# Performance work log

Hardware: AMD Instinct MI355X
Metric: run time of the kernel (lower is better)

The kernel has to match this reference:

```python
import jax, jax.numpy as jnp
import numpy as np

B = 32768
H = 320          # pred_hidden
V = 34           # num_classes
BLANK = V - 1    # padding_idx for embedding


def setup_inputs() -> dict:
    key = jax.random.key(0)
    ks = jax.random.split(key, 12)
    s = 0.05
    embed_W = jax.random.normal(ks[0], (V, H), jnp.float32) * s
    embed_W = embed_W.at[BLANK].set(0.0)  # padding_idx row is zeros in torch
    return {
        "x": jax.random.randint(ks[1], (B,), 0, V, jnp.int32),
        "enc_proj_line": jax.random.normal(ks[2], (B, H), jnp.float32),
        "h": jax.random.normal(ks[3], (1, B, H), jnp.float32),
        "c": jax.random.normal(ks[4], (1, B, H), jnp.float32),
        "embed_W": embed_W,
        "W_ih": jax.random.normal(ks[5], (4 * H, H), jnp.float32) * s,
        "W_hh": jax.random.normal(ks[6], (4 * H, H), jnp.float32) * s,
        "b_ih": jax.random.normal(ks[7], (4 * H,), jnp.float32) * s,
        "b_hh": jax.random.normal(ks[8], (4 * H,), jnp.float32) * s,
        "pred_W": jax.random.normal(ks[9], (H, H), jnp.float32) * s,
        "pred_b": jnp.zeros((H,), jnp.float32),
        "joint_W": jax.random.normal(ks[10], (V, H), jnp.float32) * s,
        "joint_b": jnp.zeros((V,), jnp.float32),
    }


def reference(x, enc_proj_line, h, c, embed_W, W_ih, W_hh, b_ih, b_hh,
              pred_W, pred_b, joint_W, joint_b):
    # embedding lookup: [B, H]
    emb = embed_W[x]
    # single-timestep LSTM cell (torch gate order: i, f, g, o)
    gates = emb @ W_ih.T + b_ih + h[0] @ W_hh.T + b_hh  # [B, 4H]
    i, f, g, o = jnp.split(gates, 4, axis=-1)
    i = jax.nn.sigmoid(i)
    f = jax.nn.sigmoid(f)
    g = jnp.tanh(g)
    o = jax.nn.sigmoid(o)
    c_new = f * c[0] + i * g                 # [B, H]
    h_new = o * jnp.tanh(c_new)              # [B, H] == g[0] (lstm output)
    # pred projection + joint
    pred_proj = h_new @ pred_W.T + pred_b    # [B, H]
    joint_out = (enc_proj_line + pred_proj) @ joint_W.T + joint_b  # [B, V]
    dec = jnp.argmax(joint_out, axis=-1)
    return dec, h_new[None], c_new[None]
```

## Files before the change

### kernel.cpp

```cpp
#include <hip/hip_runtime.h>
#include <math.h>

#define NB 32768
#define H 320
#define V 34
#define N4 1280
#define BM 128
#define BN 128
#define BK 32
#define KSTEPS (H / BK)
#define NWG ((NB / BM) * (N4 / BN))

typedef _Float16 f16;
typedef f16 f16x4 __attribute__((ext_vector_type(4)));
typedef f16 f16x8 __attribute__((ext_vector_type(8)));
typedef float f32x4 __attribute__((ext_vector_type(4)));

#define WS_GTP 0
#define WS_C2 43520
#define WS_JB2 54400
#define WS_HALF_BYTE 217744
#define WP_COUNT (N4 * H)
#define WS_JP_BYTE 1856144
#define JP_COUNT (48 * 640)
#define BUILD_T0 43520
#define BUILD_T1 54400
#define BUILD_T2 54434
#define BUILD_TOTAL (BUILD_T2 + WP_COUNT)

#define JBM 64
#define JBN 48
#define JBK 32
#define JKSTEPS 20

__device__ __forceinline__ float sigf(float x) {
    return 1.0f / (1.0f + __expf(-x));
}
__device__ __forceinline__ float tanh_fast(float x) {
    return 1.0f - 2.0f / (1.0f + __expf(2.0f * x));
}

__global__ void build_tables(const float* __restrict__ embed_W,
                             const float* __restrict__ W_ih,
                             const float* __restrict__ b_ih,
                             const float* __restrict__ b_hh,
                             const float* __restrict__ pred_W,
                             const float* __restrict__ pred_b,
                             const float* __restrict__ joint_W,
                             const float* __restrict__ joint_b,
                             const float* __restrict__ W_hh,
                             float* __restrict__ ws) {
    int tid = blockIdx.x * blockDim.x + threadIdx.x;
    if (tid < BUILD_T0) {
        int v = tid / N4, n = tid % N4;
        int orig = (n & 3) * H + (n >> 2);
        float acc = b_ih[orig] + b_hh[orig];
        const float* e = embed_W + (size_t)v * H;
        const float* w = W_ih + (size_t)orig * H;
        for (int k = 0; k < H; k += 4) {
            float4 e4 = *(const float4*)(e + k);
            float4 w4 = *(const float4*)(w + k);
            acc = fmaf(e4.x, w4.x, acc);
            acc = fmaf(e4.y, w4.y, acc);
            acc = fmaf(e4.z, w4.z, acc);
            acc = fmaf(e4.w, w4.w, acc);
        }
        ws[WS_GTP + tid] = acc;
    } else if (tid < BUILD_T1) {
        int idx = tid - BUILD_T0;
        int v = idx / H, k = idx % H;
        float acc = 0.0f;
        for (int j = 0; j < H; ++j)
            acc = fmaf(joint_W[(size_t)v * H + j], pred_W[(size_t)j * H + k], acc);
        ws[tid] = acc;
    } else if (tid < BUILD_T2) {
        int v = tid - BUILD_T1;
        float acc = joint_b[v];
        for (int j = 0; j < H; ++j)
            acc = fmaf(joint_W[(size_t)v * H + j], pred_b[j], acc);
        ws[tid] = acc;
    } else if (tid < BUILD_TOTAL) {
        int idx = tid - BUILD_T2;
        int n = idx / H, k = idx % H;
        int orig = (n & 3) * H + (n >> 2);
        float wv = W_hh[(size_t)orig * H + k];
        f16 w1 = (f16)wv;
        f16 w2 = (f16)((wv - (float)w1) * 2048.0f);
        f16* wp1 = (f16*)((char*)ws + WS_HALF_BYTE);
        wp1[idx] = w1;
        wp1[WP_COUNT + idx] = w2;
    }
}

__global__ void build_joint(const float* __restrict__ joint_W,
                            float* __restrict__ ws) {
    int tid = blockIdx.x * blockDim.x + threadIdx.x;
    if (tid >= JP_COUNT) return;
    int n = tid / 640, k = tid % 640;
    float wv = 0.0f;
    if (n < V)
        wv = (k < H) ? joint_W[(size_t)n * H + k] : ws[WS_C2 + (size_t)n * H + (k - H)];
    f16 w1 = (f16)wv;
    f16 w2 = (f16)((wv - (float)w1) * 2048.0f);
    f16* jp1 = (f16*)((char*)ws + WS_JP_BYTE);
    jp1[tid] = w1;
    jp1[JP_COUNT + tid] = w2;
}

__device__ __forceinline__ void stage_tile(int w, int lane, int m0, int n0, int kc,
                                           const float* __restrict__ h_in,
                                           const f16* __restrict__ Wp1,
                                           const f16* __restrict__ Wp2,
                                           f16* A1, f16* A2, f16* B1, f16* B2) {
    #pragma unroll
    for (int i = 0; i < 4; ++i) {
        int r = (w * 4 + i) * 8 + (lane >> 3);
        int cf = (lane & 7) * 4;
        float4 hv = *(const float4*)(h_in + (size_t)(m0 + r) * H + kc + cf);
        f16x4 h1v, h2v;
        f16 a;
        a = (f16)hv.x; h1v[0] = a; h2v[0] = (f16)((hv.x - (float)a) * 2048.0f);
        a = (f16)hv.y; h1v[1] = a; h2v[1] = (f16)((hv.y - (float)a) * 2048.0f);
        a = (f16)hv.z; h1v[2] = a; h2v[2] = (f16)((hv.z - (float)a) * 2048.0f);
        a = (f16)hv.w; h1v[3] = a; h2v[3] = (f16)((hv.w - (float)a) * 2048.0f);
        *(f16x4*)(A1 + r * 32 + cf) = h1v;
        *(f16x4*)(A2 + r * 32 + cf) = h2v;
    }
    #pragma unroll
    for (int i = 0; i < 2; ++i) {
        int nrow = (w * 2 + i) * 16 + (lane >> 2);
        int kh = (lane & 3) * 8;
        *(int4*)(B1 + nrow * 32 + kh) =
            *(const int4*)(Wp1 + (size_t)(n0 + nrow) * H + kc + kh);
        *(int4*)(B2 + nrow * 32 + kh) =
            *(const int4*)(Wp2 + (size_t)(n0 + nrow) * H + kc + kh);
    }
}

__launch_bounds__(256, 2)
__global__ void lstm_gemm(const int* __restrict__ x,
                          const float* __restrict__ h_in,
                          const float* __restrict__ c_in,
                          const float* __restrict__ ws,
                          float* __restrict__ out) {
    __shared__ __align__(16) char smem[65536];
    const int tid = threadIdx.x, lane = tid & 63, w = tid >> 6;

    int l = (blockIdx.x & 7) * (NWG / 8) + (blockIdx.x >> 3);
    const int mb = l / (N4 / BN);
    const int nb = l % (N4 / BN);
    const int m0 = mb * BM, n0 = nb * BN;

    const f16* Wp1 = (const f16*)((const char*)ws + WS_HALF_BYTE);
    const f16* Wp2 = Wp1 + WP_COUNT;
    const float* gtp = ws + WS_GTP;
    float* hn_out = out + NB;
    float* cn_out = out + NB + (size_t)NB * H;

    f16* base = (f16*)smem;

    f32x4 accM[4][4], accC[4][4];
    #pragma unroll
    for (int i = 0; i < 4; ++i)
        #pragma unroll
        for (int j = 0; j < 4; ++j) {
            accM[i][j] = (f32x4){0.f, 0.f, 0.f, 0.f};
            accC[i][j] = (f32x4){0.f, 0.f, 0.f, 0.f};
        }

    stage_tile(w, lane, m0, n0, 0, h_in, Wp1, Wp2,
               base, base + 4096, base + 8192, base + 12288);
    __syncthreads();

    const int wm = (w >> 1) * 64, wn = (w & 1) * 64;
    int cur = 0;
    for (int t = 0; t < KSTEPS; ++t) {
        if (t < KSTEPS - 1) {
            f16* nb_ = base + (cur ^ 1) * 16384;
            stage_tile(w, lane, m0, n0, (t + 1) * BK, h_in, Wp1, Wp2,
                       nb_, nb_ + 4096, nb_ + 8192, nb_ + 12288);
        }
        f16* A1 = base + cur * 16384;
        f16* A2 = A1 + 4096;
        f16* B1 = A1 + 8192;
        f16* B2 = A1 + 12288;
        const int ar = (lane & 15) * 32 + (lane >> 4) * 8;

        f16x8 a[4], b1[4], b2[4];
        #pragma unroll
        for (int mi = 0; mi < 4; ++mi)
            a[mi] = *(const f16x8*)(A1 + (wm + mi * 16) * 32 + ar);
        #pragma unroll
        for (int nj = 0; nj < 4; ++nj)
            b1[nj] = *(const f16x8*)(B1 + (wn + nj * 16) * 32 + ar);
        #pragma unroll
        for (int mi = 0; mi < 4; ++mi)
            #pragma unroll
            for (int nj = 0; nj < 4; ++nj)
                accM[mi][nj] = __builtin_amdgcn_mfma_f32_16x16x32_f16(
                    a[mi], b1[nj], accM[mi][nj], 0, 0, 0);
        #pragma unroll
        for (int nj = 0; nj < 4; ++nj)
            b2[nj] = *(const f16x8*)(B2 + (wn + nj * 16) * 32 + ar);
        #pragma unroll
        for (int mi = 0; mi < 4; ++mi)
            #pragma unroll
            for (int nj = 0; nj < 4; ++nj)
                accC[mi][nj] = __builtin_amdgcn_mfma_f32_16x16x32_f16(
                    a[mi], b2[nj], accC[mi][nj], 0, 0, 0);
        #pragma unroll
        for (int mi = 0; mi < 4; ++mi)
            a[mi] = *(const f16x8*)(A2 + (wm + mi * 16) * 32 + ar);
        #pragma unroll
        for (int mi = 0; mi < 4; ++mi)
            #pragma unroll
            for (int nj = 0; nj < 4; ++nj)
                accC[mi][nj] = __builtin_amdgcn_mfma_f32_16x16x32_f16(
                    a[mi], b1[nj], accC[mi][nj], 0, 0, 0);
        __syncthreads();
        cur ^= 1;
    }

    float* gates = (float*)smem;
    #pragma unroll
    for (int mi = 0; mi < 4; ++mi)
        #pragma unroll
        for (int nj = 0; nj < 4; ++nj) {
            f32x4 vm = accM[mi][nj];
            f32x4 vc = accC[mi][nj];
            int n = wn + nj * 16 + (lane & 15);
            int mb4 = wm + mi * 16 + (lane >> 4) * 4;
            #pragma unroll
            for (int q = 0; q < 4; ++q)
                gates[(mb4 + q) * 128 + n] = fmaf(vc[q], 1.0f / 2048.0f, vm[q]);
        }
    __syncthreads();

    const int hk0 = n0 >> 2;
    #pragma unroll 4
    for (int it = 0; it < 16; ++it) {
        int idx = it * 256 + tid;
        int ml = idx >> 5, hkl = idx & 31;
        f32x4 g4 = *(const f32x4*)&gates[ml * 128 + hkl * 4];
        int m = m0 + ml;
        int hk = hk0 + hkl;
        int xv = x[m];
        float4 b4 = *(const float4*)(gtp + (size_t)xv * N4 + n0 + hkl * 4);
        float ig = sigf(g4[0] + b4.x);
        float fg = sigf(g4[1] + b4.y);
        float gg = tanh_fast(g4[2] + b4.z);
        float og = sigf(g4[3] + b4.w);
        float cv = c_in[(size_t)m * H + hk];
        float cn = fmaf(fg, cv, ig * gg);
        float hn = og * tanh_fast(cn);
        hn_out[(size_t)m * H + hk] = hn;
        cn_out[(size_t)m * H + hk] = cn;
    }
}

__launch_bounds__(256, 2)
__global__ void joint_argmax(const float* __restrict__ enc,
                             const float* __restrict__ ws,
                             float* __restrict__ out) {
    __shared__ __align__(16) char smem[28672];
    const int tid = threadIdx.x, lane = tid & 63, w = tid >> 6;
    const int m0 = blockIdx.x * JBM;

    const f16* Jp1 = (const f16*)((const char*)ws + WS_JP_BYTE);
    const f16* Jp2 = Jp1 + JP_COUNT;
    const float* hn = out + NB;
    const float* jb2 = ws + WS_JB2;

    f16* base = (f16*)smem;

    f32x4 accM[3], accC[3];
    #pragma unroll
    for (int j = 0; j < 3; ++j) {
        accM[j] = (f32x4){0.f, 0.f, 0.f, 0.f};
        accC[j] = (f32x4){0.f, 0.f, 0.f, 0.f};
    }

    auto stage = [&](int t, f16* A1, f16* A2, f16* B1, f16* B2) {
        const float* src = (t < 10) ? enc : hn;
        const int off = (t % 10) * JBK;
        #pragma unroll
        for (int i = 0; i < 2; ++i) {
            int r = (w * 2 + i) * 8 + (lane >> 3);
            int cf = (lane & 7) * 4;
            float4 hv = *(const float4*)(src + (size_t)(m0 + r) * H + off + cf);
            f16x4 h1v, h2v;
            f16 a;
            a = (f16)hv.x; h1v[0] = a; h2v[0] = (f16)((hv.x - (float)a) * 2048.0f);
            a = (f16)hv.y; h1v[1] = a; h2v[1] = (f16)((hv.y - (float)a) * 2048.0f);
            a = (f16)hv.z; h1v[2] = a; h2v[2] = (f16)((hv.z - (float)a) * 2048.0f);
            a = (f16)hv.w; h1v[3] = a; h2v[3] = (f16)((hv.w - (float)a) * 2048.0f);
            *(f16x4*)(A1 + r * 32 + cf) = h1v;
            *(f16x4*)(A2 + r * 32 + cf) = h2v;
        }
        if (tid < 192) {
            int n = tid >> 2, kh = (tid & 3) * 8;
            size_t gsrc = (size_t)n * 640 + t * JBK + kh;
            *(int4*)(B1 + n * 32 + kh) = *(const int4*)(Jp1 + gsrc);
            *(int4*)(B2 + n * 32 + kh) = *(const int4*)(Jp2 + gsrc);
        }
    };

    stage(0, base, base + 2048, base + 4096, base + 5632);
    __syncthreads();

    const int wm = w * 16;
    int cur = 0;
    for (int t = 0; t < JKSTEPS; ++t) {
        if (t < JKSTEPS - 1) {
            f16* nb_ = base + (cur ^ 1) * 7168;
            stage(t + 1, nb_, nb_ + 2048, nb_ + 4096, nb_ + 5632);
        }
        f16* A1 = base + cur * 7168;
        f16* A2 = A1 + 2048;
        f16* B1 = A1 + 4096;
        f16* B2 = A1 + 5632;
        const int ar = (lane & 15) * 32 + (lane >> 4) * 8;

        f16x8 a1 = *(const f16x8*)(A1 + wm * 32 + ar);
        f16x8 a2 = *(const f16x8*)(A2 + wm * 32 + ar);
        f16x8 b1[3], b2[3];
        #pragma unroll
        for (int nj = 0; nj < 3; ++nj) {
            b1[nj] = *(const f16x8*)(B1 + nj * 16 * 32 + ar);
            b2[nj] = *(const f16x8*)(B2 + nj * 16 * 32 + ar);
        }
        #pragma unroll
        for (int nj = 0; nj < 3; ++nj) {
            accM[nj] = __builtin_amdgcn_mfma_f32_16x16x32_f16(a1, b1[nj], accM[nj], 0, 0, 0);
            accC[nj] = __builtin_amdgcn_mfma_f32_16x16x32_f16(a1, b2[nj], accC[nj], 0, 0, 0);
            accC[nj] = __builtin_amdgcn_mfma_f32_16x16x32_f16(a2, b1[nj], accC[nj], 0, 0, 0);
        }
        __syncthreads();
        cur ^= 1;
    }

    float* lg = (float*)smem;
    #pragma unroll
    for (int nj = 0; nj < 3; ++nj) {
        int n = nj * 16 + (lane & 15);
        int mr = wm + (lane >> 4) * 4;
        #pragma unroll
        for (int q = 0; q < 4; ++q)
            lg[(mr + q) * 49 + n] = fmaf(accC[nj][q], 1.0f / 2048.0f, accM[nj][q]);
    }
    __syncthreads();

    if (tid < JBM) {
        const float* row = lg + tid * 49;
        float best = row[0] + jb2[0];
        int bi = 0;
        #pragma unroll
        for (int v = 1; v < V; ++v) {
            float t2 = row[v] + jb2[v];
            if (t2 > best) { best = t2; bi = v; }
        }
        out[m0 + tid] = (float)bi;
    }
}

extern "C" void kernel_launch(void* const* d_in, const int* in_sizes, int n_in,
                              void* d_out, int out_size, void* d_ws, size_t ws_size,
                              hipStream_t stream) {
    const int*   x       = (const int*)  d_in[0];
    const float* enc     = (const float*)d_in[1];
    const float* h       = (const float*)d_in[2];
    const float* c       = (const float*)d_in[3];
    const float* embed_W = (const float*)d_in[4];
    const float* W_ih    = (const float*)d_in[5];
    const float* W_hh    = (const float*)d_in[6];
    const float* b_ih    = (const float*)d_in[7];
    const float* b_hh    = (const float*)d_in[8];
    const float* pred_W  = (const float*)d_in[9];
    const float* pred_b  = (const float*)d_in[10];
    const float* joint_W = (const float*)d_in[11];
    const float* joint_b = (const float*)d_in[12];
    float* out = (float*)d_out;
    float* ws  = (float*)d_ws;

    int tblocks = (BUILD_TOTAL + 255) / 256;
    build_tables<<<tblocks, 256, 0, stream>>>(embed_W, W_ih, b_ih, b_hh,
                                              pred_W, pred_b, joint_W, joint_b,
                                              W_hh, ws);
    build_joint<<<(JP_COUNT + 255) / 256, 256, 0, stream>>>(joint_W, ws);
    lstm_gemm<<<NWG, 256, 0, stream>>>(x, h, c, ws, out);
    joint_argmax<<<NB / JBM, 256, 0, stream>>>(enc, ws, out);
}
```

Baseline: 166.0 us.

## Pre-split h into tiled fp16 pairs and stage GEMM tiles via global_load_lds

Adds a split_h kernel that converts h into hi/lo fp16 pairs once, stored in a tile-contiguous layout in the workspace. W_hh is also stored tile-contiguous. A new lstm_gemm_fast kernel stages A and B tiles straight into LDS with global_load_lds, with each wave copying one contiguous 8KB block, so the GEMM no longer converts fp32 to fp16 per tile or goes through registers. The cost is an extra kernel launch plus writing and re-reading about 42MB of split h. The fast path is used only when the workspace is large enough, otherwise the old kernel runs.

```diff
diff --git a/kernel.cpp b/kernel.cpp
--- a/kernel.cpp
+++ b/kernel.cpp
@@ -19,14 +19,18 @@
 #define WS_GTP 0
 #define WS_C2 43520
 #define WS_JB2 54400
-#define WS_HALF_BYTE 217744
-#define WP_COUNT (N4 * H)
+#define WS_B_BYTE 217744
+#define BT_COUNT (N4 * H)
 #define WS_JP_BYTE 1856144
 #define JP_COUNT (48 * 640)
+#define WS_AT_BYTE 1979136
+#define AT_COUNT (NB * H)
+#define FAST_WS_NEED (WS_AT_BYTE + 2ull * AT_COUNT * 2)
+
 #define BUILD_T0 43520
 #define BUILD_T1 54400
 #define BUILD_T2 54434
-#define BUILD_TOTAL (BUILD_T2 + WP_COUNT)
+#define BUILD_TOTAL (BUILD_T2 + BT_COUNT)
 
 #define JBM 64
 #define JBN 48
@@ -39,6 +43,9 @@
 __device__ __forceinline__ float tanh_fast(float x) {
     return 1.0f - 2.0f / (1.0f + __expf(2.0f * x));
 }
+
+typedef const __attribute__((address_space(1))) unsigned int* gas_t;
+typedef __attribute__((address_space(3))) unsigned int* las_t;
 
 __global__ void build_tables(const float* __restrict__ embed_W,
                              const float* __restrict__ W_ih,
@@ -86,9 +93,10 @@
         float wv = W_hh[(size_t)orig * H + k];
         f16 w1 = (f16)wv;
         f16 w2 = (f16)((wv - (float)w1) * 2048.0f);
-        f16* wp1 = (f16*)((char*)ws + WS_HALF_BYTE);
-        wp1[idx] = w1;
-        wp1[WP_COUNT + idx] = w2;
+        int off = ((n >> 7) * KSTEPS + (k >> 5)) * 4096 + (n & 127) * 32 + (k & 31);
+        f16* bt1 = (f16*)((char*)ws + WS_B_BYTE);
+        bt1[off] = w1;
+        bt1[BT_COUNT + off] = w2;
     }
 }
 
@@ -107,11 +115,161 @@
     jp1[JP_COUNT + tid] = w2;
 }
 
-__device__ __forceinline__ void stage_tile(int w, int lane, int m0, int n0, int kc,
+__global__ void split_h(const float* __restrict__ h_in, float* __restrict__ ws) {
+    int tid = blockIdx.x * blockDim.x + threadIdx.x;
+    int e = tid * 4;
+    int m = e / H, k = e % H;
+    float4 hv = *(const float4*)(h_in + e);
+    f16x4 h1v, h2v;
+    f16 a;
+    a = (f16)hv.x; h1v[0] = a; h2v[0] = (f16)((hv.x - (float)a) * 2048.0f);
+    a = (f16)hv.y; h1v[1] = a; h2v[1] = (f16)((hv.y - (float)a) * 2048.0f);
+    a = (f16)hv.z; h1v[2] = a; h2v[2] = (f16)((hv.z - (float)a) * 2048.0f);
+    a = (f16)hv.w; h1v[3] = a; h2v[3] = (f16)((hv.w - (float)a) * 2048.0f);
+    int off = ((m >> 7) * KSTEPS + (k >> 5)) * 4096 + (m & 127) * 32 + (k & 31);
+    f16* at1 = (f16*)((char*)ws + WS_AT_BYTE);
+    *(f16x4*)(at1 + off) = h1v;
+    *(f16x4*)(at1 + AT_COUNT + off) = h2v;
+}
+
+__launch_bounds__(256, 2)
+__global__ void lstm_gemm_fast(const int* __restrict__ x,
+                               const float* __restrict__ c_in,
+                               const float* __restrict__ ws,
+                               float* __restrict__ out) {
+    __shared__ __align__(16) char smem[65536];
+    const int tid = threadIdx.x, lane = tid & 63, w = tid >> 6;
+
+    int l = (blockIdx.x & 7) * (NWG / 8) + (blockIdx.x >> 3);
+    const int mb = l / (N4 / BN);
+    const int nb = l % (N4 / BN);
+    const int m0 = mb * BM, n0 = nb * BN;
+
+    const f16* At1 = (const f16*)((const char*)ws + WS_AT_BYTE);
+    const f16* Bt1 = (const f16*)((const char*)ws + WS_B_BYTE);
+    const float* gtp = ws + WS_GTP;
+    float* hn_out = out + NB;
+    float* cn_out = out + NB + (size_t)NB * H;
+
+    f32x4 accM[4][4], accC[4][4];
+    #pragma unroll
+    for (int i = 0; i < 4; ++i)
+        #pragma unroll
+        for (int j = 0; j < 4; ++j) {
+            accM[i][j] = (f32x4){0.f, 0.f, 0.f, 0.f};
+            accC[i][j] = (f32x4){0.f, 0.f, 0.f, 0.f};
+        }
+
+    auto stage = [&](int ks, int buf) {
+        const f16* src;
+        if (w == 0)      src = At1 + (size_t)(mb * KSTEPS + ks) * 4096;
+        else if (w == 1) src = At1 + AT_COUNT + (size_t)(mb * KSTEPS + ks) * 4096;
+        else if (w == 2) src = Bt1 + (size_t)(nb * KSTEPS + ks) * 4096;
+        else             src = Bt1 + BT_COUNT + (size_t)(nb * KSTEPS + ks) * 4096;
+        char* ldst = smem + buf * 32768 + w * 8192;
+        #pragma unroll
+        for (int i = 0; i < 8; ++i) {
+            __builtin_amdgcn_global_load_lds(
+                (gas_t)(const void*)(src + i * 512 + lane * 8),
+                (las_t)(void*)(ldst + i * 1024), 16, 0, 0);
+        }
+    };
+
+    stage(0, 0);
+    __syncthreads();
+
+    const int wm = (w >> 1) * 64, wn = (w & 1) * 64;
+    const int ar = (lane & 15) * 32 + (lane >> 4) * 8;
+    int cur = 0;
+    for (int t = 0; t < KSTEPS; ++t) {
+        if (t < KSTEPS - 1) stage(t + 1, cur ^ 1);
+        const f16* A1 = (const f16*)(smem + cur * 32768);
+        const f16* A2 = A1 + 4096;
+        const f16* B1 = A1 + 8192;
+        const f16* B2 = A1 + 12288;
+
+        f16x8 a[4], b1[4], b2[4];
+        #pragma unroll
+        for (int mi = 0; mi < 4; ++mi)
+            a[mi] = *(const f16x8*)(A1 + (wm + mi * 16) * 32 + ar);
+        #pragma unroll
+        for (int nj = 0; nj < 4; ++nj)
+            b1[nj] = *(const f16x8*)(B1 + (wn + nj * 16) * 32 + ar);
+        #pragma unroll
+        for (int mi = 0; mi < 4; ++mi)
+            #pragma unroll
+            for (int nj = 0; nj < 4; ++nj)
+                accM[mi][nj] = __builtin_amdgcn_mfma_f32_16x16x32_f16(
+                    a[mi], b1[nj], accM[mi][nj], 0, 0, 0);
+        #pragma unroll
+        for (int nj = 0; nj < 4; ++nj)
+            b2[nj] = *(const f16x8*)(B2 + (wn + nj * 16) * 32 + ar);
+        #pragma unroll
+        for (int mi = 0; mi < 4; ++mi)
+            #pragma unroll
+            for (int nj = 0; nj < 4; ++nj)
+                accC[mi][nj] = __builtin_amdgcn_mfma_f32_16x16x32_f16(
+                    a[mi], b2[nj], accC[mi][nj], 0, 0, 0);
+        #pragma unroll
+        for (int mi = 0; mi < 4; ++mi)
+            a[mi] = *(const f16x8*)(A2 + (wm + mi * 16) * 32 + ar);
+        #pragma unroll
+        for (int mi = 0; mi < 4; ++mi)
+            #pragma unroll
+            for (int nj = 0; nj < 4; ++nj)
+                accC[mi][nj] = __builtin_amdgcn_mfma_f32_16x16x32_f16(
+                    a[mi], b1[nj], accC[mi][nj], 0, 0, 0);
+        __syncthreads();
+        cur ^= 1;
+    }
+
+    float* gates = (float*)smem;
+    #pragma unroll
+    for (int mi = 0; mi < 4; ++mi)
+        #pragma unroll
+        for (int nj = 0; nj < 4; ++nj) {
+            f32x4 vm = accM[mi][nj];
+            f32x4 vc = accC[mi][nj];
+            int n = wn + nj * 16 + (lane & 15);
+            int mb4 = wm + mi * 16 + (lane >> 4) * 4;
+            #pragma unroll
+            for (int q = 0; q < 4; ++q) {
+                int row = mb4 + q;
+                gates[row * 128 + (n ^ ((row & 7) << 2))] =
+                    fmaf(vc[q], 1.0f / 2048.0f, vm[q]);
+            }
+        }
+    __syncthreads();
+
+    const int hk0 = n0 >> 2;
+    #pragma unroll 4
+    for (int it = 0; it < 16; ++it) {
+        int idx = it * 256 + tid;
+        int ml = idx >> 5, hkl = idx & 31;
+        int k0 = (ml & 7) << 2;
+        f32x4 g4 = *(const f32x4*)&gates[ml * 128 + ((hkl * 4) ^ k0)];
+        int m = m0 + ml;
+        int hk = hk0 + hkl;
+        int xv = x[m];
+        float4 b4 = *(const float4*)(gtp + (size_t)xv * N4 + n0 + hkl * 4);
+        float ig = sigf(g4[0] + b4.x);
+        float fg = sigf(g4[1] + b4.y);
+        float gg = tanh_fast(g4[2] + b4.z);
+        float og = sigf(g4[3] + b4.w);
+        float cv = c_in[(size_t)m * H + hk];
+        float cn = fmaf(fg, cv, ig * gg);
+        float hn = og * tanh_fast(cn);
+        hn_out[(size_t)m * H + hk] = hn;
+        cn_out[(size_t)m * H + hk] = cn;
+    }
+}
+
+__device__ __forceinline__ void stage_tile(int w, int lane, int m0, int nb, int ks,
                                            const float* __restrict__ h_in,
-                                           const f16* __restrict__ Wp1,
-                                           const f16* __restrict__ Wp2,
+                                           const f16* __restrict__ Bt1,
+                                           const f16* __restrict__ Bt2,
                                            f16* A1, f16* A2, f16* B1, f16* B2) {
+    int kc = ks * BK;
     #pragma unroll
     for (int i = 0; i < 4; ++i) {
         int r = (w * 4 + i) * 8 + (lane >> 3);
@@ -130,10 +288,9 @@
     for (int i = 0; i < 2; ++i) {
         int nrow = (w * 2 + i) * 16 + (lane >> 2);
         int kh = (lane & 3) * 8;
-        *(int4*)(B1 + nrow * 32 + kh) =
-            *(const int4*)(Wp1 + (size_t)(n0 + nrow) * H + kc + kh);
-        *(int4*)(B2 + nrow * 32 + kh) =
-            *(const int4*)(Wp2 + (size_t)(n0 + nrow) * H + kc + kh);
+        size_t src = (size_t)(nb * KSTEPS + ks) * 4096 + nrow * 32 + kh;
+        *(int4*)(B1 + nrow * 32 + kh) = *(const int4*)(Bt1 + src);
+        *(int4*)(B2 + nrow * 32 + kh) = *(const int4*)(Bt2 + src);
     }
 }
 
@@ -151,8 +308,8 @@
     const int nb = l % (N4 / BN);
     const int m0 = mb * BM, n0 = nb * BN;
 
-    const f16* Wp1 = (const f16*)((const char*)ws + WS_HALF_BYTE);
-    const f16* Wp2 = Wp1 + WP_COUNT;
+    const f16* Bt1 = (const f16*)((const char*)ws + WS_B_BYTE);
+    const f16* Bt2 = Bt1 + BT_COUNT;
     const float* gtp = ws + WS_GTP;
     float* hn_out = out + NB;
     float* cn_out = out + NB + (size_t)NB * H;
@@ -168,7 +325,7 @@
             accC[i][j] = (f32x4){0.f, 0.f, 0.f, 0.f};
         }
 
-    stage_tile(w, lane, m0, n0, 0, h_in, Wp1, Wp2,
+    stage_tile(w, lane, m0, nb, 0, h_in, Bt1, Bt2,
                base, base + 4096, base + 8192, base + 12288);
     __syncthreads();
 
@@ -177,7 +334,7 @@
     for (int t = 0; t < KSTEPS; ++t) {
         if (t < KSTEPS - 1) {
             f16* nb_ = base + (cur ^ 1) * 16384;
-            stage_tile(w, lane, m0, n0, (t + 1) * BK, h_in, Wp1, Wp2,
+            stage_tile(w, lane, m0, nb, t + 1, h_in, Bt1, Bt2,
                        nb_, nb_ + 4096, nb_ + 8192, nb_ + 12288);
         }
         f16* A1 = base + cur * 16384;
@@ -387,6 +544,12 @@
                                               pred_W, pred_b, joint_W, joint_b,
                                               W_hh, ws);
     build_joint<<<(JP_COUNT + 255) / 256, 256, 0, stream>>>(joint_W, ws);
-    lstm_gemm<<<NWG, 256, 0, stream>>>(x, h, c, ws, out);
+
+    if (ws_size >= FAST_WS_NEED) {
+        split_h<<<(AT_COUNT / 4) / 256, 256, 0, stream>>>(h, ws);
+        lstm_gemm_fast<<<NWG, 256, 0, stream>>>(x, c, ws, out);
+    } else {
+        lstm_gemm<<<NWG, 256, 0, stream>>>(x, h, c, ws, out);
+    }
     joint_argmax<<<NB / JBM, 256, 0, stream>>>(enc, ws, out);
 }
```

New measurement: 171.2 us. +3.1%, slower.

## Pre-split h and W_hh into MFMA-tiled fp16 layouts, stage via global_load_lds

Applied to the files above, without the earlier changes.

A merged prep kernel now splits h and W_hh into hi/lo fp16 pairs, stored in tile-contiguous layouts that match the MFMA fragment order. The LSTM GEMM then stages tiles straight into LDS with global_load_lds, so it no longer converts in-loop or issues register round-trips. It also folds build_joint into prep, swizzles the gate scratch in LDS to avoid bank conflicts, and retiles the joint weight layout. The trade-off is an extra full pass over h (write and reread of 2x fp16 copies, about 42MB) in exchange for a simpler, faster main loop.

```diff
diff --git a/kernel.cpp b/kernel.cpp
--- a/kernel.cpp
+++ b/kernel.cpp
@@ -17,22 +17,24 @@
 typedef float f32x4 __attribute__((ext_vector_type(4)));
 
 #define WS_GTP 0
-#define WS_C2 43520
 #define WS_JB2 54400
-#define WS_HALF_BYTE 217744
-#define WP_COUNT (N4 * H)
+#define WS_B_BYTE 217744
+#define BT_COUNT (N4 * H)
 #define WS_JP_BYTE 1856144
 #define JP_COUNT (48 * 640)
-#define BUILD_T0 43520
-#define BUILD_T1 54400
-#define BUILD_T2 54434
-#define BUILD_TOTAL (BUILD_T2 + WP_COUNT)
+#define WS_AT_BYTE 1979136
+#define AT_COUNT (NB * H)
 
 #define JBM 64
-#define JBN 48
 #define JBK 32
 #define JKSTEPS 20
 
+#define PREP_P4 1280
+#define PREP_P2 50
+#define PREP_P0 170
+#define PREP_P3 120
+#define PREP_NWG (PREP_P4 + PREP_P2 + PREP_P0 + PREP_P3 + 1)
+
 __device__ __forceinline__ float sigf(float x) {
     return 1.0f / (1.0f + __expf(-x));
 }
@@ -40,19 +42,71 @@
     return 1.0f - 2.0f / (1.0f + __expf(2.0f * x));
 }
 
-__global__ void build_tables(const float* __restrict__ embed_W,
-                             const float* __restrict__ W_ih,
-                             const float* __restrict__ b_ih,
-                             const float* __restrict__ b_hh,
-                             const float* __restrict__ pred_W,
-                             const float* __restrict__ pred_b,
-                             const float* __restrict__ joint_W,
-                             const float* __restrict__ joint_b,
-                             const float* __restrict__ W_hh,
-                             float* __restrict__ ws) {
-    int tid = blockIdx.x * blockDim.x + threadIdx.x;
-    if (tid < BUILD_T0) {
-        int v = tid / N4, n = tid % N4;
+typedef const __attribute__((address_space(1))) unsigned int* gas_t;
+typedef __attribute__((address_space(3))) unsigned int* las_t;
+
+__device__ __forceinline__ void split8(const float* e, f16x8& p1, f16x8& p2) {
+    #pragma unroll
+    for (int j = 0; j < 8; ++j) {
+        f16 a = (f16)e[j];
+        p1[j] = a;
+        p2[j] = (f16)((e[j] - (float)a) * 2048.0f);
+    }
+}
+
+__global__ void prep(const float* __restrict__ embed_W,
+                     const float* __restrict__ W_ih,
+                     const float* __restrict__ b_ih,
+                     const float* __restrict__ b_hh,
+                     const float* __restrict__ pred_W,
+                     const float* __restrict__ pred_b,
+                     const float* __restrict__ joint_W,
+                     const float* __restrict__ joint_b,
+                     const float* __restrict__ W_hh,
+                     const float* __restrict__ h_in,
+                     float* __restrict__ ws) {
+    const int bid = blockIdx.x;
+    const int t = threadIdx.x;
+    if (bid < PREP_P4) {
+        int id = bid * 256 + t;
+        int ks = id >> 15, m = id & 32767;
+        const float* src = h_in + (size_t)m * H + ks * 32;
+        f16* at1 = (f16*)((char*)ws + WS_AT_BYTE);
+        f16* at2 = at1 + AT_COUNT;
+        size_t tbase = ((size_t)(m >> 7) * KSTEPS + ks) * 4096
+                       + ((m & 127) >> 4) * 512 + (m & 15) * 8;
+        #pragma unroll
+        for (int g = 0; g < 4; ++g) {
+            float4 v0 = *(const float4*)(src + g * 8);
+            float4 v1 = *(const float4*)(src + g * 8 + 4);
+            float e[8] = {v0.x, v0.y, v0.z, v0.w, v1.x, v1.y, v1.z, v1.w};
+            f16x8 p1, p2;
+            split8(e, p1, p2);
+            *(f16x8*)(at1 + tbase + g * 128) = p1;
+            *(f16x8*)(at2 + tbase + g * 128) = p2;
+        }
+    } else if (bid < PREP_P4 + PREP_P2) {
+        int id = (bid - PREP_P4) * 256 + t;
+        int ks = id / 1280, n = id - ks * 1280;
+        int orig = (n & 3) * H + (n >> 2);
+        const float* src = W_hh + (size_t)orig * H + ks * 32;
+        f16* bt1 = (f16*)((char*)ws + WS_B_BYTE);
+        f16* bt2 = bt1 + BT_COUNT;
+        size_t tbase = ((size_t)(n >> 7) * KSTEPS + ks) * 4096
+                       + ((n & 127) >> 4) * 512 + (n & 15) * 8;
+        #pragma unroll
+        for (int g = 0; g < 4; ++g) {
+            float4 v0 = *(const float4*)(src + g * 8);
+            float4 v1 = *(const float4*)(src + g * 8 + 4);
+            float e[8] = {v0.x, v0.y, v0.z, v0.w, v1.x, v1.y, v1.z, v1.w};
+            f16x8 p1, p2;
+            split8(e, p1, p2);
+            *(f16x8*)(bt1 + tbase + g * 128) = p1;
+            *(f16x8*)(bt2 + tbase + g * 128) = p2;
+        }
+    } else if (bid < PREP_P4 + PREP_P2 + PREP_P0) {
+        int id = (bid - PREP_P4 - PREP_P2) * 256 + t;
+        int v = id / N4, n = id % N4;
         int orig = (n & 3) * H + (n >> 2);
         float acc = b_ih[orig] + b_hh[orig];
         const float* e = embed_W + (size_t)v * H;
@@ -65,84 +119,46 @@
             acc = fmaf(e4.z, w4.z, acc);
             acc = fmaf(e4.w, w4.w, acc);
         }
-        ws[WS_GTP + tid] = acc;
-    } else if (tid < BUILD_T1) {
-        int idx = tid - BUILD_T0;
-        int v = idx / H, k = idx % H;
-        float acc = 0.0f;
-        for (int j = 0; j < H; ++j)
-            acc = fmaf(joint_W[(size_t)v * H + j], pred_W[(size_t)j * H + k], acc);
-        ws[tid] = acc;
-    } else if (tid < BUILD_T2) {
-        int v = tid - BUILD_T1;
-        float acc = joint_b[v];
-        for (int j = 0; j < H; ++j)
-            acc = fmaf(joint_W[(size_t)v * H + j], pred_b[j], acc);
-        ws[tid] = acc;
-    } else if (tid < BUILD_TOTAL) {
-        int idx = tid - BUILD_T2;
-        int n = idx / H, k = idx % H;
-        int orig = (n & 3) * H + (n >> 2);
-        float wv = W_hh[(size_t)orig * H + k];
+        ws[WS_GTP + id] = acc;
+    } else if (bid < PREP_P4 + PREP_P2 + PREP_P0 + PREP_P3) {
+        int id = (bid - PREP_P4 - PREP_P2 - PREP_P0) * 256 + t;
+        int n = id / 640, k = id % 640;
+        float wv = 0.0f;
+        if (n < V) {
+            if (k < H) {
+                wv = joint_W[(size_t)n * H + k];
+            } else {
+                float acc = 0.0f;
+                const float* jw = joint_W + (size_t)n * H;
+                for (int j = 0; j < H; ++j)
+                    acc = fmaf(jw[j], pred_W[(size_t)j * H + (k - H)], acc);
+                wv = acc;
+            }
+        }
         f16 w1 = (f16)wv;
         f16 w2 = (f16)((wv - (float)w1) * 2048.0f);
-        f16* wp1 = (f16*)((char*)ws + WS_HALF_BYTE);
-        wp1[idx] = w1;
-        wp1[WP_COUNT + idx] = w2;
-    }
-}
-
-__global__ void build_joint(const float* __restrict__ joint_W,
-                            float* __restrict__ ws) {
-    int tid = blockIdx.x * blockDim.x + threadIdx.x;
-    if (tid >= JP_COUNT) return;
-    int n = tid / 640, k = tid % 640;
-    float wv = 0.0f;
-    if (n < V)
-        wv = (k < H) ? joint_W[(size_t)n * H + k] : ws[WS_C2 + (size_t)n * H + (k - H)];
-    f16 w1 = (f16)wv;
-    f16 w2 = (f16)((wv - (float)w1) * 2048.0f);
-    f16* jp1 = (f16*)((char*)ws + WS_JP_BYTE);
-    jp1[tid] = w1;
-    jp1[JP_COUNT + tid] = w2;
-}
-
-__device__ __forceinline__ void stage_tile(int w, int lane, int m0, int n0, int kc,
-                                           const float* __restrict__ h_in,
-                                           const f16* __restrict__ Wp1,
-                                           const f16* __restrict__ Wp2,
-                                           f16* A1, f16* A2, f16* B1, f16* B2) {
-    #pragma unroll
-    for (int i = 0; i < 4; ++i) {
-        int r = (w * 4 + i) * 8 + (lane >> 3);
-        int cf = (lane & 7) * 4;
-        float4 hv = *(const float4*)(h_in + (size_t)(m0 + r) * H + kc + cf);
-        f16x4 h1v, h2v;
-        f16 a;
-        a = (f16)hv.x; h1v[0] = a; h2v[0] = (f16)((hv.x - (float)a) * 2048.0f);
-        a = (f16)hv.y; h1v[1] = a; h2v[1] = (f16)((hv.y - (float)a) * 2048.0f);
-        a = (f16)hv.z; h1v[2] = a; h2v[2] = (f16)((hv.z - (float)a) * 2048.0f);
-        a = (f16)hv.w; h1v[3] = a; h2v[3] = (f16)((hv.w - (float)a) * 2048.0f);
-        *(f16x4*)(A1 + r * 32 + cf) = h1v;
-        *(f16x4*)(A2 + r * 32 + cf) = h2v;
-    }
-    #pragma unroll
-    for (int i = 0; i < 2; ++i) {
-        int nrow = (w * 2 + i) * 16 + (lane >> 2);
-        int kh = (lane & 3) * 8;
-        *(int4*)(B1 + nrow * 32 + kh) =
-            *(const int4*)(Wp1 + (size_t)(n0 + nrow) * H + kc + kh);
-        *(int4*)(B2 + nrow * 32 + kh) =
-            *(const int4*)(Wp2 + (size_t)(n0 + nrow) * H + kc + kh);
+        int kk = k & 31;
+        int off = (k >> 5) * 1536 + (n >> 4) * 512 + (kk >> 3) * 128
+                  + (n & 15) * 8 + (kk & 7);
+        f16* jp1 = (f16*)((char*)ws + WS_JP_BYTE);
+        jp1[off] = w1;
+        jp1[JP_COUNT + off] = w2;
+    } else {
+        if (t < V) {
+            float acc = joint_b[t];
+            const float* jw = joint_W + (size_t)t * H;
+            for (int j = 0; j < H; ++j)
+                acc = fmaf(jw[j], pred_b[j], acc);
+            ws[WS_JB2 + t] = acc;
+        }
     }
 }
 
 __launch_bounds__(256, 2)
-__global__ void lstm_gemm(const int* __restrict__ x,
-                          const float* __restrict__ h_in,
-                          const float* __restrict__ c_in,
-                          const float* __restrict__ ws,
-                          float* __restrict__ out) {
+__global__ void lstm_gemm_fast(const int* __restrict__ x,
+                               const float* __restrict__ c_in,
+                               const float* __restrict__ ws,
+                               float* __restrict__ out) {
     __shared__ __align__(16) char smem[65536];
     const int tid = threadIdx.x, lane = tid & 63, w = tid >> 6;
 
@@ -151,14 +167,12 @@
     const int nb = l % (N4 / BN);
     const int m0 = mb * BM, n0 = nb * BN;
 
-    const f16* Wp1 = (const f16*)((const char*)ws + WS_HALF_BYTE);
-    const f16* Wp2 = Wp1 + WP_COUNT;
+    const f16* At1 = (const f16*)((const char*)ws + WS_AT_BYTE);
+    const f16* Bt1 = (const f16*)((const char*)ws + WS_B_BYTE);
     const float* gtp = ws + WS_GTP;
     float* hn_out = out + NB;
     float* cn_out = out + NB + (size_t)NB * H;
 
-    f16* base = (f16*)smem;
-
     f32x4 accM[4][4], accC[4][4];
     #pragma unroll
     for (int i = 0; i < 4; ++i)
@@ -168,31 +182,42 @@
             accC[i][j] = (f32x4){0.f, 0.f, 0.f, 0.f};
         }
 
-    stage_tile(w, lane, m0, n0, 0, h_in, Wp1, Wp2,
-               base, base + 4096, base + 8192, base + 12288);
+    auto stage = [&](int ks, int buf) {
+        const f16* src;
+        if (w == 0)      src = At1 + (size_t)(mb * KSTEPS + ks) * 4096;
+        else if (w == 1) src = At1 + AT_COUNT + (size_t)(mb * KSTEPS + ks) * 4096;
+        else if (w == 2) src = Bt1 + (size_t)(nb * KSTEPS + ks) * 4096;
+        else             src = Bt1 + BT_COUNT + (size_t)(nb * KSTEPS + ks) * 4096;
+        char* ldst = smem + buf * 32768 + w * 8192;
+        #pragma unroll
+        for (int i = 0; i < 8; ++i) {
+            __builtin_amdgcn_global_load_lds(
+                (gas_t)(const void*)(src + i * 512 + lane * 8),
+                (las_t)(void*)(ldst + i * 1024), 16, 0, 0);
+        }
+    };
+
+    stage(0, 0);
     __syncthreads();
 
-    const int wm = (w >> 1) * 64, wn = (w & 1) * 64;
+    const int asub = (w >> 1) * 4;
+    const int bsub = (w & 1) * 4;
+    const int lo = lane * 8;
     int cur = 0;
     for (int t = 0; t < KSTEPS; ++t) {
-        if (t < KSTEPS - 1) {
-            f16* nb_ = base + (cur ^ 1) * 16384;
-            stage_tile(w, lane, m0, n0, (t + 1) * BK, h_in, Wp1, Wp2,
-                       nb_, nb_ + 4096, nb_ + 8192, nb_ + 12288);
-        }
-        f16* A1 = base + cur * 16384;
-        f16* A2 = A1 + 4096;
-        f16* B1 = A1 + 8192;
-        f16* B2 = A1 + 12288;
-        const int ar = (lane & 15) * 32 + (lane >> 4) * 8;
+        if (t < KSTEPS - 1) stage(t + 1, cur ^ 1);
+        const f16* A1 = (const f16*)(smem + cur * 32768);
+        const f16* A2 = A1 + 4096;
+        const f16* B1 = A1 + 8192;
+        const f16* B2 = A1 + 12288;
 
         f16x8 a[4], b1[4], b2[4];
         #pragma unroll
         for (int mi = 0; mi < 4; ++mi)
-            a[mi] = *(const f16x8*)(A1 + (wm + mi * 16) * 32 + ar);
+            a[mi] = *(const f16x8*)(A1 + (asub + mi) * 512 + lo);
         #pragma unroll
         for (int nj = 0; nj < 4; ++nj)
-            b1[nj] = *(const f16x8*)(B1 + (wn + nj * 16) * 32 + ar);
+            b1[nj] = *(const f16x8*)(B1 + (bsub + nj) * 512 + lo);
         #pragma unroll
         for (int mi = 0; mi < 4; ++mi)
             #pragma unroll
@@ -201,7 +226,7 @@
                     a[mi], b1[nj], accM[mi][nj], 0, 0, 0);
         #pragma unroll
         for (int nj = 0; nj < 4; ++nj)
-            b2[nj] = *(const f16x8*)(B2 + (wn + nj * 16) * 32 + ar);
+            b2[nj] = *(const f16x8*)(B2 + (bsub + nj) * 512 + lo);
         #pragma unroll
         for (int mi = 0; mi < 4; ++mi)
             #pragma unroll
@@ -210,7 +235,7 @@
                     a[mi], b2[nj], accC[mi][nj], 0, 0, 0);
         #pragma unroll
         for (int mi = 0; mi < 4; ++mi)
-            a[mi] = *(const f16x8*)(A2 + (wm + mi * 16) * 32 + ar);
+            a[mi] = *(const f16x8*)(A2 + (asub + mi) * 512 + lo);
         #pragma unroll
         for (int mi = 0; mi < 4; ++mi)
             #pragma unroll
@@ -221,6 +246,7 @@
         cur ^= 1;
     }
 
+    const int wm = (w >> 1) * 64, wn = (w & 1) * 64;
     float* gates = (float*)smem;
     #pragma unroll
     for (int mi = 0; mi < 4; ++mi)
@@ -231,8 +257,11 @@
             int n = wn + nj * 16 + (lane & 15);
             int mb4 = wm + mi * 16 + (lane >> 4) * 4;
             #pragma unroll
-            for (int q = 0; q < 4; ++q)
-                gates[(mb4 + q) * 128 + n] = fmaf(vc[q], 1.0f / 2048.0f, vm[q]);
+            for (int q = 0; q < 4; ++q) {
+                int row = mb4 + q;
+                gates[row * 128 + (n ^ ((row & 7) << 2))] =
+                    fmaf(vc[q], 1.0f / 2048.0f, vm[q]);
+            }
         }
     __syncthreads();
 
@@ -241,7 +270,8 @@
     for (int it = 0; it < 16; ++it) {
         int idx = it * 256 + tid;
         int ml = idx >> 5, hkl = idx & 31;
-        f32x4 g4 = *(const f32x4*)&gates[ml * 128 + hkl * 4];
+        int k0 = (ml & 7) << 2;
+        f32x4 g4 = *(const f32x4*)&gates[ml * 128 + ((hkl * 4) ^ k0)];
         int m = m0 + ml;
         int hk = hk0 + hkl;
         int xv = x[m];
@@ -281,34 +311,28 @@
     }
 
     auto stage = [&](int t, f16* A1, f16* A2, f16* B1, f16* B2) {
-        const float* src = (t < 10) ? enc : hn;
-        const int off = (t % 10) * JBK;
-        #pragma unroll
-        for (int i = 0; i < 2; ++i) {
-            int r = (w * 2 + i) * 8 + (lane >> 3);
-            int cf = (lane & 7) * 4;
-            float4 hv = *(const float4*)(src + (size_t)(m0 + r) * H + off + cf);
-            f16x4 h1v, h2v;
-            f16 a;
-            a = (f16)hv.x; h1v[0] = a; h2v[0] = (f16)((hv.x - (float)a) * 2048.0f);
-            a = (f16)hv.y; h1v[1] = a; h2v[1] = (f16)((hv.y - (float)a) * 2048.0f);
-            a = (f16)hv.z; h1v[2] = a; h2v[2] = (f16)((hv.z - (float)a) * 2048.0f);
-            a = (f16)hv.w; h1v[3] = a; h2v[3] = (f16)((hv.w - (float)a) * 2048.0f);
-            *(f16x4*)(A1 + r * 32 + cf) = h1v;
-            *(f16x4*)(A2 + r * 32 + cf) = h2v;
-        }
+        const float* srcp = (t < 10) ? enc : hn;
+        const int koff = (t % 10) * JBK;
+        int row = (tid >> 6) * 16 + (tid & 15);
+        int k0 = ((tid & 63) >> 4) * 8;
+        const float* sp = srcp + (size_t)(m0 + row) * H + koff + k0;
+        float4 v0 = *(const float4*)sp;
+        float4 v1 = *(const float4*)(sp + 4);
+        float e[8] = {v0.x, v0.y, v0.z, v0.w, v1.x, v1.y, v1.z, v1.w};
+        f16x8 p1, p2;
+        split8(e, p1, p2);
+        *(f16x8*)(A1 + tid * 8) = p1;
+        *(f16x8*)(A2 + tid * 8) = p2;
         if (tid < 192) {
-            int n = tid >> 2, kh = (tid & 3) * 8;
-            size_t gsrc = (size_t)n * 640 + t * JBK + kh;
-            *(int4*)(B1 + n * 32 + kh) = *(const int4*)(Jp1 + gsrc);
-            *(int4*)(B2 + n * 32 + kh) = *(const int4*)(Jp2 + gsrc);
+            *(int4*)(B1 + tid * 8) = *(const int4*)(Jp1 + t * 1536 + tid * 8);
+            *(int4*)(B2 + tid * 8) = *(const int4*)(Jp2 + t * 1536 + tid * 8);
         }
     };
 
     stage(0, base, base + 2048, base + 4096, base + 5632);
     __syncthreads();
 
-    const int wm = w * 16;
+    const int lo = lane * 8;
     int cur = 0;
     for (int t = 0; t < JKSTEPS; ++t) {
         if (t < JKSTEPS - 1) {
@@ -319,15 +343,14 @@
         f16* A2 = A1 + 2048;
         f16* B1 = A1 + 4096;
         f16* B2 = A1 + 5632;
-        const int ar = (lane & 15) * 32 + (lane >> 4) * 8;
-
-        f16x8 a1 = *(const f16x8*)(A1 + wm * 32 + ar);
-        f16x8 a2 = *(const f16x8*)(A2 + wm * 32 + ar);
+
+        f16x8 a1 = *(const f16x8*)(A1 + w * 512 + lo);
+        f16x8 a2 = *(const f16x8*)(A2 + w * 512 + lo);
         f16x8 b1[3], b2[3];
         #pragma unroll
         for (int nj = 0; nj < 3; ++nj) {
-            b1[nj] = *(const f16x8*)(B1 + nj * 16 * 32 + ar);
-            b2[nj] = *(const f16x8*)(B2 + nj * 16 * 32 + ar);
+            b1[nj] = *(const f16x8*)(B1 + nj * 512 + lo);
+            b2[nj] = *(const f16x8*)(B2 + nj * 512 + lo);
         }
         #pragma unroll
         for (int nj = 0; nj < 3; ++nj) {
@@ -340,6 +363,7 @@
     }
 
     float* lg = (float*)smem;
+    const int wm = w * 16;
     #pragma unroll
     for (int nj = 0; nj < 3; ++nj) {
         int n = nj * 16 + (lane & 15);
@@ -382,11 +406,9 @@
     float* out = (float*)d_out;
     float* ws  = (float*)d_ws;
 
-    int tblocks = (BUILD_TOTAL + 255) / 256;
-    build_tables<<<tblocks, 256, 0, stream>>>(embed_W, W_ih, b_ih, b_hh,
-                                              pred_W, pred_b, joint_W, joint_b,
-                                              W_hh, ws);
-    build_joint<<<(JP_COUNT + 255) / 256, 256, 0, stream>>>(joint_W, ws);
-    lstm_gemm<<<NWG, 256, 0, stream>>>(x, h, c, ws, out);
+    prep<<<PREP_NWG, 256, 0, stream>>>(embed_W, W_ih, b_ih, b_hh,
+                                       pred_W, pred_b, joint_W, joint_b,
+                                       W_hh, h, ws);
+    lstm_gemm_fast<<<NWG, 256, 0, stream>>>(x, c, ws, out);
     joint_argmax<<<NB / JBM, 256, 0, stream>>>(enc, ws, out);
 }
```

Result: no change. 163.3 us (-1.7%).
